# Kernel tuning notes

Measured on AMD Instinct MI355X. Metric: run time of the kernel, lower is better.

Reference implementation:

```python
import jax, jax.numpy as jnp
import numpy as np

NUM_USERS = 100000
NUM_ITEMS = 100000
EMBED_F = 64
BATCH = 8192
MAX_HIST = 200
MU = 3.5


def setup_inputs() -> dict:
    key = jax.random.key(0)
    ks = jax.random.split(key, 9)
    inv_f = 1.0 / EMBED_F
    return {
        "user": jax.random.randint(ks[0], (BATCH,), 0, NUM_USERS),
        "item": jax.random.randint(ks[1], (BATCH,), 0, NUM_ITEMS),
        "implicit": jax.random.randint(ks[2], (BATCH, MAX_HIST), 0, NUM_ITEMS),
        "hist_len": jax.random.randint(ks[3], (BATCH,), 0, MAX_HIST),
        "P": jax.random.normal(ks[4], (NUM_USERS, EMBED_F), dtype=jnp.float32) * inv_f,
        "Q": jax.random.normal(ks[5], (NUM_ITEMS, EMBED_F), dtype=jnp.float32) * inv_f,
        "Y": jax.random.normal(ks[6], (NUM_ITEMS, EMBED_F), dtype=jnp.float32) * inv_f,
        "bu": jax.random.normal(ks[7], (NUM_USERS,), dtype=jnp.float32),
        "bi": jax.random.normal(ks[8], (NUM_ITEMS,), dtype=jnp.float32),
    }


def reference(user, item, implicit, hist_len, P, Q, Y, bu, bi):
    # lengths clamped to >=1 (original assumes every user has implicit feedback)
    lengths = jnp.maximum(hist_len, 1)                      # [B]
    mask = (jnp.arange(MAX_HIST)[None, :] < lengths[:, None]).astype(P.dtype)  # [B,H]

    # baseline estimate: mu + b_u + b_i
    bui = MU + bu[user] + bi[item]                          # [B]

    P_u = P[user]                                           # [B,F]
    Q_i = Q[item]                                           # [B,F]

    # ragged embedding-bag sum over implicit items (masked gather+sum)
    Y_g = Y[implicit]                                       # [B,H,F]
    y_sum = jnp.einsum("bhf,bh->bf", Y_g, mask)             # [B,F]
    norm = lengths.astype(P.dtype) ** -0.5                  # [B]

    rui = bui + jnp.sum(P_u * (Q_i + norm[:, None] * y_sum), axis=1)
    return rui
```

## Files before the change

### kernel.cpp

```cpp
#include <hip/hip_runtime.h>

#define BATCH_SZ 8192
#define MAX_HIST 200
#define EMBED_F 64

__device__ __forceinline__ float4 f4add(float4 a, float4 b) {
    return make_float4(a.x + b.x, a.y + b.y, a.z + b.z, a.w + b.w);
}

__global__ __launch_bounds__(256) void svdpp_kernel(
    const int*   __restrict__ user,
    const int*   __restrict__ item,
    const int*   __restrict__ implicit,
    const int*   __restrict__ hist_len,
    const float* __restrict__ P,
    const float* __restrict__ Q,
    const float* __restrict__ Y,
    const float* __restrict__ bu,
    const float* __restrict__ bi,
    float*       __restrict__ out)
{
    __shared__ int lds_idx[4][MAX_HIST];

    const int wblk = (int)(threadIdx.x >> 6);
    const int b    = (int)(blockIdx.x * 4 + wblk);
    const int lane = (int)(threadIdx.x & 63);
    const int g = lane >> 4;
    const int s = lane & 15;

    const int L = max(hist_len[b], 1);

    const int u  = user[b];
    const int it = item[b];
    const float4 pu = reinterpret_cast<const float4*>(P)[(size_t)u  * 16 + s];
    const float4 qi = reinterpret_cast<const float4*>(Q)[(size_t)it * 16 + s];
    const float bub = bu[u];
    const float bib = bi[it];

    const int* idx_row = implicit + (size_t)b * MAX_HIST;
    if (lane < MAX_HIST / 4) {
        int4 v = *reinterpret_cast<const int4*>(idx_row + lane * 4);
        *reinterpret_cast<int4*>(&lds_idx[wblk][lane * 4]) = v;
    }
    __syncthreads();

    const int* myidx = lds_idx[wblk];
    const float4* __restrict__ Y4 = reinterpret_cast<const float4*>(Y);

    float4 acc = make_float4(0.f, 0.f, 0.f, 0.f);
    int h = 0;

    for (; h + 64 <= L; h += 64) {
        float4 y[16];
        #pragma unroll
        for (int j = 0; j < 16; ++j) {
            const int i = myidx[h + j * 4 + g];
            y[j] = Y4[(size_t)i * 16 + s];
        }
        float4 t0 = f4add(f4add(f4add(y[0], y[1]),  f4add(y[2], y[3])),
                          f4add(f4add(y[4], y[5]),  f4add(y[6], y[7])));
        float4 t1 = f4add(f4add(f4add(y[8], y[9]),  f4add(y[10], y[11])),
                          f4add(f4add(y[12], y[13]), f4add(y[14], y[15])));
        acc = f4add(acc, f4add(t0, t1));
    }
    for (; h + 16 <= L; h += 16) {
        const int i0 = myidx[h      + g];
        const int i1 = myidx[h + 4  + g];
        const int i2 = myidx[h + 8  + g];
        const int i3 = myidx[h + 12 + g];
        const float4 y0 = Y4[(size_t)i0 * 16 + s];
        const float4 y1 = Y4[(size_t)i1 * 16 + s];
        const float4 y2 = Y4[(size_t)i2 * 16 + s];
        const float4 y3 = Y4[(size_t)i3 * 16 + s];
        acc = f4add(acc, f4add(f4add(y0, y1), f4add(y2, y3)));
    }
    for (; h < L; h += 4) {
        const int i = myidx[h + g];
        const float4 y = Y4[(size_t)i * 16 + s];
        if (h + g < L) acc = f4add(acc, y);
    }

    #pragma unroll
    for (int off = 16; off < 64; off <<= 1) {
        acc.x += __shfl_xor(acc.x, off, 64);
        acc.y += __shfl_xor(acc.y, off, 64);
        acc.z += __shfl_xor(acc.z, off, 64);
        acc.w += __shfl_xor(acc.w, off, 64);
    }

    const float norm = 1.0f / sqrtf((float)L);
    float v = pu.x * (qi.x + norm * acc.x)
            + pu.y * (qi.y + norm * acc.y)
            + pu.z * (qi.z + norm * acc.z)
            + pu.w * (qi.w + norm * acc.w);

    #pragma unroll
    for (int off = 1; off < 16; off <<= 1)
        v += __shfl_xor(v, off, 64);

    if (lane == 0)
        out[b] = 3.5f + bub + bib + v;
}

extern "C" void kernel_launch(void* const* d_in, const int* in_sizes, int n_in,
                              void* d_out, int out_size, void* d_ws, size_t ws_size,
                              hipStream_t stream) {
    const int*   user     = (const int*)  d_in[0];
    const int*   item     = (const int*)  d_in[1];
    const int*   implicit = (const int*)  d_in[2];
    const int*   hist_len = (const int*)  d_in[3];
    const float* P        = (const float*)d_in[4];
    const float* Q        = (const float*)d_in[5];
    const float* Y        = (const float*)d_in[6];
    const float* bu       = (const float*)d_in[7];
    const float* bi       = (const float*)d_in[8];
    float* out = (float*)d_out;

    const int threads = 256;
    const int blocks  = BATCH_SZ / 4;
    svdpp_kernel<<<blocks, threads, 0, stream>>>(
        user, item, implicit, hist_len, P, Q, Y, bu, bi, out);
}
```

Measured before the change: 135.9 us.

## Split each batch row's history gather across two wavefronts

Each block now handles one batch row with two wavefronts, where the old layout put four rows in a block with one wavefront per row. The two wavefronts interleave 4-row history packs, and their partial sums are combined through LDS before the final dot product. The aim is to raise memory-level parallelism and balance work, since history lengths vary between rows. The cost is an extra __syncthreads, an LDS reduction, and a smaller unroll depth per wavefront.

```diff
diff --git a/kernel.cpp b/kernel.cpp
--- a/kernel.cpp
+++ b/kernel.cpp
@@ -8,7 +8,7 @@
     return make_float4(a.x + b.x, a.y + b.y, a.z + b.z, a.w + b.w);
 }
 
-__global__ __launch_bounds__(256) void svdpp_kernel(
+__global__ __launch_bounds__(128) void svdpp_kernel(
     const int*   __restrict__ user,
     const int*   __restrict__ item,
     const int*   __restrict__ implicit,
@@ -20,64 +20,68 @@
     const float* __restrict__ bi,
     float*       __restrict__ out)
 {
-    __shared__ int lds_idx[4][MAX_HIST];
+    __shared__ int    lds_idx[MAX_HIST];
+    __shared__ float4 lds_part[16];
 
-    const int wblk = (int)(threadIdx.x >> 6);
-    const int b    = (int)(blockIdx.x * 4 + wblk);
+    const int b    = (int)blockIdx.x;
+    const int w    = (int)(threadIdx.x >> 6);
     const int lane = (int)(threadIdx.x & 63);
     const int g = lane >> 4;
     const int s = lane & 15;
 
     const int L = max(hist_len[b], 1);
 
-    const int u  = user[b];
-    const int it = item[b];
-    const float4 pu = reinterpret_cast<const float4*>(P)[(size_t)u  * 16 + s];
-    const float4 qi = reinterpret_cast<const float4*>(Q)[(size_t)it * 16 + s];
-    const float bub = bu[u];
-    const float bib = bi[it];
+    int u = 0, it = 0;
+    float4 pu = make_float4(0.f, 0.f, 0.f, 0.f);
+    float4 qi = make_float4(0.f, 0.f, 0.f, 0.f);
+    float bub = 0.f, bib = 0.f;
+    if (w == 0) {
+        u  = user[b];
+        it = item[b];
+        pu = reinterpret_cast<const float4*>(P)[(size_t)u  * 16 + s];
+        qi = reinterpret_cast<const float4*>(Q)[(size_t)it * 16 + s];
+        bub = bu[u];
+        bib = bi[it];
+    }
 
     const int* idx_row = implicit + (size_t)b * MAX_HIST;
-    if (lane < MAX_HIST / 4) {
-        int4 v = *reinterpret_cast<const int4*>(idx_row + lane * 4);
-        *reinterpret_cast<int4*>(&lds_idx[wblk][lane * 4]) = v;
+    if (threadIdx.x < MAX_HIST / 4) {
+        int4 v = *reinterpret_cast<const int4*>(idx_row + threadIdx.x * 4);
+        *reinterpret_cast<int4*>(&lds_idx[threadIdx.x * 4]) = v;
     }
     __syncthreads();
 
-    const int* myidx = lds_idx[wblk];
     const float4* __restrict__ Y4 = reinterpret_cast<const float4*>(Y);
 
+    const int full   = L >> 2;
+    const int npacks = (L + 3) >> 2;
+
     float4 acc = make_float4(0.f, 0.f, 0.f, 0.f);
-    int h = 0;
+    int p = w;
 
-    for (; h + 64 <= L; h += 64) {
-        float4 y[16];
+    for (; p + 14 < full; p += 16) {
+        float4 y[8];
         #pragma unroll
-        for (int j = 0; j < 16; ++j) {
-            const int i = myidx[h + j * 4 + g];
+        for (int j = 0; j < 8; ++j) {
+            const int i = lds_idx[4 * (p + 2 * j) + g];
             y[j] = Y4[(size_t)i * 16 + s];
         }
-        float4 t0 = f4add(f4add(f4add(y[0], y[1]),  f4add(y[2], y[3])),
-                          f4add(f4add(y[4], y[5]),  f4add(y[6], y[7])));
-        float4 t1 = f4add(f4add(f4add(y[8], y[9]),  f4add(y[10], y[11])),
-                          f4add(f4add(y[12], y[13]), f4add(y[14], y[15])));
-        acc = f4add(acc, f4add(t0, t1));
+        acc = f4add(acc, f4add(f4add(f4add(y[0], y[1]), f4add(y[2], y[3])),
+                               f4add(f4add(y[4], y[5]), f4add(y[6], y[7]))));
     }
-    for (; h + 16 <= L; h += 16) {
-        const int i0 = myidx[h      + g];
-        const int i1 = myidx[h + 4  + g];
-        const int i2 = myidx[h + 8  + g];
-        const int i3 = myidx[h + 12 + g];
-        const float4 y0 = Y4[(size_t)i0 * 16 + s];
-        const float4 y1 = Y4[(size_t)i1 * 16 + s];
-        const float4 y2 = Y4[(size_t)i2 * 16 + s];
-        const float4 y3 = Y4[(size_t)i3 * 16 + s];
-        acc = f4add(acc, f4add(f4add(y0, y1), f4add(y2, y3)));
+    for (; p + 6 < full; p += 8) {
+        float4 y[4];
+        #pragma unroll
+        for (int j = 0; j < 4; ++j) {
+            const int i = lds_idx[4 * (p + 2 * j) + g];
+            y[j] = Y4[(size_t)i * 16 + s];
+        }
+        acc = f4add(acc, f4add(f4add(y[0], y[1]), f4add(y[2], y[3])));
     }
-    for (; h < L; h += 4) {
-        const int i = myidx[h + g];
+    for (; p < npacks; p += 2) {
+        const int i = lds_idx[4 * p + g];
         const float4 y = Y4[(size_t)i * 16 + s];
-        if (h + g < L) acc = f4add(acc, y);
+        if (4 * p + g < L) acc = f4add(acc, y);
     }
 
     #pragma unroll
@@ -88,18 +92,25 @@
         acc.w += __shfl_xor(acc.w, off, 64);
     }
 
-    const float norm = 1.0f / sqrtf((float)L);
-    float v = pu.x * (qi.x + norm * acc.x)
-            + pu.y * (qi.y + norm * acc.y)
-            + pu.z * (qi.z + norm * acc.z)
-            + pu.w * (qi.w + norm * acc.w);
+    if (w == 1 && lane < 16) lds_part[s] = acc;
+    __syncthreads();
+    if (w == 0) {
+        const float4 o = lds_part[s];
+        acc = f4add(acc, o);
 
-    #pragma unroll
-    for (int off = 1; off < 16; off <<= 1)
-        v += __shfl_xor(v, off, 64);
+        const float norm = 1.0f / sqrtf((float)L);
+        float v = pu.x * (qi.x + norm * acc.x)
+                + pu.y * (qi.y + norm * acc.y)
+                + pu.z * (qi.z + norm * acc.z)
+                + pu.w * (qi.w + norm * acc.w);
 
-    if (lane == 0)
-        out[b] = 3.5f + bub + bib + v;
+        #pragma unroll
+        for (int off = 1; off < 16; off <<= 1)
+            v += __shfl_xor(v, off, 64);
+
+        if (lane == 0)
+            out[b] = 3.5f + bub + bib + v;
+    }
 }
 
 extern "C" void kernel_launch(void* const* d_in, const int* in_sizes, int n_in,
@@ -116,8 +127,6 @@
     const float* bi       = (const float*)d_in[8];
     float* out = (float*)d_out;
 
-    const int threads = 256;
-    const int blocks  = BATCH_SZ / 4;
-    svdpp_kernel<<<blocks, threads, 0, stream>>>(
+    svdpp_kernel<<<BATCH_SZ, 128, 0, stream>>>(
         user, item, implicit, hist_len, P, Q, Y, bu, bi, out);
 }
```

After: 135.6 us. Within noise of the previous version (-0.2%).
